# Kernel tuning notes

Hardware: AMD Instinct MI355X
Metric: run time of the kernel (lower is better)

The kernel has to match this reference:

```python
import jax, jax.numpy as jnp
import numpy as np

N, K, D, E, H = 65536, 8, 256, 256, 132  # points, components, latent_dim, encoder_dim, FC hidden

def setup_inputs() -> dict:
    key = jax.random.key(0)
    ks = jax.random.split(key, 12)
    s = 0.05
    f32 = jnp.float32
    return {
        "signal": jax.random.normal(ks[0], (N, E), f32),
        "components": jax.random.normal(ks[1], (K, N, D), f32),
        # message_map / update_map: Linear(D, D)
        "Wm": jax.random.normal(ks[2], (D, D), f32) * s,
        "bm": jnp.zeros((D,), f32),
        "Wu": jax.random.normal(ks[3], (D, D), f32) * s,
        "bu": jnp.zeros((D,), f32),
        "W0": jax.random.normal(ks[4], (H, E + D), f32) * s,
        "b0": jnp.zeros((H,), f32),
        "W1": jax.random.normal(ks[5], (H, H), f32) * s,
        "b1": jnp.zeros((H,), f32),
        "W2": jax.random.normal(ks[6], (H, H), f32) * s,
        "b2": jnpes if False else jnp.zeros((H,), f32),
        "W3": jax.random.normal(ks[7], (D, H), f32) * s,
        "b3": jnp.zeros((D,), f32),
    }

def reference(signal, components, Wm, bm, Wu, bu, W0, b0, W1, b1, W2, b2, W3, b3):
    k = components.shape[0]
    # sum_k Linear(comp_k) == Linear applied to sum, with bias counted k times (linearity)
    right = components.sum(0) @ Wm.T + k * bm          # [N, D]
    right = right @ Wu.T + bu                          # update_map
    x = jnp.concatenate([signal, right], axis=-1)      # [N, E+D]
    x = jax.nn.relu(x @ W0.T + b0)
    x = jax.nn.relu(x @ W1.T + b1)
    x = jax.nn.relu(x @ W2.T + b2)
    return x @ W3.T + b3                               # [N, D]
```

## Files before the change

kernel.cpp:

```cpp
#include <hip/hip_runtime.h>
#include <hip/hip_bf16.h>


typedef float  f32x4  __attribute__((ext_vector_type(4)));
typedef __bf16 bf16x8 __attribute__((ext_vector_type(8)));
typedef unsigned int   u32x2 __attribute__((ext_vector_type(2)));
typedef unsigned short u16x8 __attribute__((ext_vector_type(8)));

__device__ __forceinline__ unsigned short f2bf(float f) {
  unsigned int u = __builtin_bit_cast(unsigned int, f);
  u += 0x7fffu + ((u >> 16) & 1u);
  return (unsigned short)(u >> 16);
}

__device__ __forceinline__ u32x2 pack4(f32x4 v) {
  u32x2 r;
  r[0] = (unsigned)f2bf(v[0]) | ((unsigned)f2bf(v[1]) << 16);
  r[1] = (unsigned)f2bf(v[2]) | ((unsigned)f2bf(v[3]) << 16);
  return r;
}

__device__ __forceinline__ float wave_reduce(float s) {
#pragma unroll
  for (int m = 32; m > 0; m >>= 1) s += __shfl_xor(s, m, 64);
  return s;
}

__device__ __forceinline__ void gl16(const void* g, void* l) {
  __builtin_amdgcn_global_load_lds(
      (const __attribute__((address_space(1))) unsigned*)(unsigned long long)g,
      (__attribute__((address_space(3))) unsigned*)(unsigned)(unsigned long long)l,
      16, 0, 0);
}
__device__ __forceinline__ void gl4(const void* g, void* l) {
  __builtin_amdgcn_global_load_lds(
      (const __attribute__((address_space(1))) unsigned*)(unsigned long long)g,
      (__attribute__((address_space(3))) unsigned*)(unsigned)(unsigned long long)l,
      4, 0, 0);
}

__device__ __forceinline__ void stage10k(const char* src, char* dst,
                                         int wave, int lane) {
  const char* g0 = src + wave * 1024 + lane * 16;
  char* l0 = dst + wave * 1024;
  gl16(g0, l0);
  gl16(g0 + 4096, l0 + 4096);
  const char* g1 = src + 8192 + wave * 256 + lane * 4;
  char* l1 = dst + 8192 + wave * 256;
  gl4(g1, l1);
  gl4(g1 + 1024, l1 + 1024);
}
__device__ __forceinline__ void stage6k(const char* src, char* dst,
                                        int wave, int lane) {
  gl16(src + wave * 1024 + lane * 16, dst + wave * 1024);
  const char* g1 = src + 4096 + wave * 256 + lane * 4;
  char* l1 = dst + 4096 + wave * 256;
  gl4(g1, l1);
  gl4(g1 + 1024, l1 + 1024);
}

__global__ __launch_bounds__(256) void kA(const float* __restrict__ comp,
                                          const float* __restrict__ W0,
                                          const float* __restrict__ Wu,
                                          const float* __restrict__ bm,
                                          const float* __restrict__ bu,
                                          float* __restrict__ U,
                                          float* __restrict__ rb,
                                          unsigned short* __restrict__ csum) {
  const int b = blockIdx.x;
  if (b >= 196) {
    const int cb = b - 196;
    const int t = threadIdx.x;
    const f32x4* cp = (const f32x4*)comp;
    const size_t base = (size_t)cb * 2048 + t;
    f32x4 a[8];
#pragma unroll
    for (int j = 0; j < 8; ++j) a[j] = cp[base + j * 256];
#pragma unroll
    for (int k = 1; k < 8; ++k) {
      f32x4 t0[8];
#pragma unroll
      for (int j = 0; j < 8; ++j) t0[j] = cp[base + (size_t)k * 4194304u + j * 256];
#pragma unroll
      for (int j = 0; j < 8; ++j) a[j] += t0[j];
    }
    u32x2* op = (u32x2*)csum;
#pragma unroll
    for (int j = 0; j < 8; ++j) op[base + j * 256] = pack4(a[j]);
  } else if (b < 132) {
    const int h = b, d = threadIdx.x;
    float s = 0.f;
#pragma unroll 8
    for (int i = 0; i < 256; ++i) s += W0[h * 512 + 256 + i] * Wu[i * 256 + d];
    U[h * 256 + d] = s;
  } else {
    const int t = (b - 132) * 4 + (threadIdx.x >> 6);
    const int lane = threadIdx.x & 63;
    f32x4 w = ((const f32x4*)(Wu + t * 256))[lane];
    f32x4 v = ((const f32x4*)bm)[lane];
    float s = w[0] * v[0] + w[1] * v[1] + w[2] * v[2] + w[3] * v[3];
    s = wave_reduce(s);
    if (lane == 0) rb[t] = 8.f * s + bu[t];
  }
}

__global__ __launch_bounds__(256) void kB(const float* __restrict__ U,
                                          const float* __restrict__ Wm,
                                          const float* __restrict__ W0,
                                          const float* __restrict__ rb,
                                          const float* __restrict__ b0,
                                          const float* __restrict__ b1,
                                          const float* __restrict__ b2,
                                          float* __restrict__ Wc,
                                          float* __restrict__ bias1,
                                          float* __restrict__ b1p,
                                          float* __restrict__ b2p) {
  const int b = blockIdx.x;
  if (b < 132) {
    const int h = b, d = threadIdx.x;
    float s = 0.f;
#pragma unroll 8
    for (int j = 0; j < 256; ++j) s += U[h * 256 + j] * Wm[j * 256 + d];
    Wc[h * 256 + d] = s;
  } else {
    const int t = (b - 132) * 4 + (threadIdx.x >> 6);
    const int lane = threadIdx.x & 63;
    float v = 0.f;
    if (t < 132) {
      f32x4 w = ((const f32x4*)(W0 + t * 512 + 256))[lane];
      f32x4 r4 = ((const f32x4*)rb)[lane];
      float s = w[0] * r4[0] + w[1] * r4[1] + w[2] * r4[2] + w[3] * r4[3];
      s = wave_reduce(s);
      v = b0[t] + s;
    }
    if (lane == 0) {
      bias1[t] = v;
      b1p[t] = (t < 132) ? b1[t] : 0.f;
      b2p[t] = (t < 132) ? b2[t] : 0.f;
    }
  }
}

__global__ __launch_bounds__(256) void kC(
    const float* __restrict__ W0, const float* __restrict__ Wc,
    const float* __restrict__ W1, const float* __restrict__ W2,
    const float* __restrict__ W3,
    unsigned short* __restrict__ P1, unsigned short* __restrict__ P2,
    unsigned short* __restrict__ P3, unsigned short* __restrict__ P4) {
  int e = blockIdx.x * 256 + threadIdx.x;
  if (e >= 174080) return;
  unsigned short* dst; int NT, rel, mode;
  if (e < 81920)       { dst = P1; NT = 10; rel = e;          mode = 0; }
  else if (e < 107520) { dst = P2; NT = 10; rel = e - 81920;  mode = 1; }
  else if (e < 133120) { dst = P3; NT = 10; rel = e - 107520; mode = 2; }
  else                 { dst = P4; NT = 16; rel = e - 133120; mode = 3; }
  int chunk = rel >> 9, q = rel & 511;
  int lane = q >> 3, j = q & 7;
  int kk = chunk / NT, nt = chunk - kk * NT;
  int k = kk * 32 + (lane >> 4) * 8 + j;
  int n = nt * 16 + (lane & 15);
  float v = 0.f;
  if (mode == 0) {
    if (n < 132) v = (k < 256) ? W0[n * 512 + k] : Wc[n * 256 + (k - 256)];
  } else if (mode == 1) {
    if (n < 132 && k < 132) v = W1[n * 132 + k];
  } else if (mode == 2) {
    if (n < 132 && k < 132) v = W2[n * 132 + k];
  } else {
    if (k < 132) v = W3[n * 132 + k];
  }
  dst[rel] = f2bf(v);
}

__global__ __launch_bounds__(256, 3) void kD(
    const float* __restrict__ signal, const unsigned short* __restrict__ csum,
    const unsigned short* __restrict__ Pseq,
    const float* __restrict__ bias1, const float* __restrict__ b1p,
    const float* __restrict__ b2p, const float* __restrict__ b3,
    float* __restrict__ out) {
  extern __shared__ char lds[];
  const int tid = threadIdx.x;
  const int wave = tid >> 6;
  const int lane = tid & 63;
  const int lhalf = lane >> 4;
  const int l16 = lane & 15;
  char* act = lds + wave * 8192;
  char* wbA = lds + 32768;
  char* wbB = lds + 32768 + 10240;
  const char* Pb = (const char*)Pseq;
  const int row0 = ((int)blockIdx.x * 4 + wave) * 16;
  const int asw = (l16 & 7) << 4;

  f32x4 sg[16];
  const f32x4* sp = (const f32x4*)signal;
#pragma unroll
  for (int r = 0; r < 16; ++r) sg[r] = sp[(size_t)(row0 + r) * 64 + lane];
  u16x8 cs[8];
  const int r2 = lane >> 5, c32 = lane & 31;
#pragma unroll
  for (int j = 0; j < 8; ++j)
    cs[j] = *(const u16x8*)(csum + (size_t)(row0 + 2 * j + r2) * 256 + c32 * 8);

#pragma unroll
  for (int r = 0; r < 16; ++r)
    *(u32x2*)(act + r * 512 + ((lane * 8) ^ ((r & 7) << 4))) = pack4(sg[r]);

  stage10k(Pb, wbA, wave, lane);
  __syncthreads();

  f32x4 acc[10];
#pragma unroll
  for (int i = 0; i < 10; ++i) acc[i] = f32x4{0.f, 0.f, 0.f, 0.f};

#pragma unroll
  for (int kk = 0; kk < 8; ++kk) {
    stage10k(Pb + (kk + 1) * 10240, (((kk + 1) & 1) ? wbB : wbA), wave, lane);
    char* wb = (kk & 1) ? wbB : wbA;
    bf16x8 af = *(const bf16x8*)(act + l16 * 512 + ((kk * 64 + lhalf * 16) ^ asw));
#pragma unroll
    for (int nt = 0; nt < 10; ++nt)
      acc[nt] = __builtin_amdgcn_mfma_f32_16x16x32_bf16(
          af, *(const bf16x8*)(wb + nt * 1024 + lane * 16), acc[nt], 0, 0, 0);
    __syncthreads();
  }

  asm volatile("" ::: "memory");
#pragma unroll
  for (int j = 0; j < 8; ++j) {
    const int rw = 2 * j + r2;
    *(u16x8*)(act + rw * 512 + ((c32 * 16) ^ ((rw & 7) << 4))) = cs[j];
  }
  asm volatile("" ::: "memory");

#pragma unroll
  for (int kk = 8; kk < 16; ++kk) {
    if (kk < 15)
      stage10k(Pb + (kk + 1) * 10240, (((kk + 1) & 1) ? wbB : wbA), wave, lane);
    else
      stage10k(Pb + 163840, wbA, wave, lane);
    char* wb = (kk & 1) ? wbB : wbA;
    bf16x8 af =
        *(const bf16x8*)(act + l16 * 512 + (((kk - 8) * 64 + lhalf * 16) ^ asw));
#pragma unroll
    for (int nt = 0; nt < 10; ++nt)
      acc[nt] = __builtin_amdgcn_mfma_f32_16x16x32_bf16(
          af, *(const bf16x8*)(wb + nt * 1024 + lane * 16), acc[nt], 0, 0, 0);
    __syncthreads();
  }

  {
    float bv[10];
#pragma unroll
    for (int nt = 0; nt < 10; ++nt) bv[nt] = bias1[nt * 16 + l16];
    asm volatile("" ::: "memory");
#pragma unroll
    for (int nt = 0; nt < 10; ++nt) {
#pragma unroll
      for (int r = 0; r < 4; ++r) {
        const int row = lhalf * 4 + r;
        float v = fmaxf(acc[nt][r] + bv[nt], 0.f);
        *(unsigned short*)(act + row * 512 +
                           (((nt * 16 + l16) * 2) ^ ((row & 7) << 4))) = f2bf(v);
      }
    }
    asm volatile("" ::: "memory");
  }

#pragma unroll
  for (int L = 0; L < 2; ++L) {
    const char* hb = Pb + (L ? 215040 : 163840);
    const float* hbias = L ? b2p : b1p;
#pragma unroll
    for (int i = 0; i < 10; ++i) acc[i] = f32x4{0.f, 0.f, 0.f, 0.f};
#pragma unroll
    for (int kk = 0; kk < 5; ++kk) {
      const char* nsrc = (kk < 4) ? (hb + (kk + 1) * 10240)
                                  : (L ? (Pb + 266240) : (Pb + 215040));
      stage10k(nsrc, (((kk + L + 1) & 1) ? wbB : wbA), wave, lane);
      char* wb = ((kk + L) & 1) ? wbB : wbA;
      bf16x8 af =
          *(const bf16x8*)(act + l16 * 512 + ((kk * 64 + lhalf * 16) ^ asw));
#pragma unroll
      for (int nt = 0; nt < 10; ++nt)
        acc[nt] = __builtin_amdgcn_mfma_f32_16x16x32_bf16(
            af, *(const bf16x8*)(wb + nt * 1024 + lane * 16), acc[nt], 0, 0, 0);
      __syncthreads();
    }
    float bv[10];
#pragma unroll
    for (int nt = 0; nt < 10; ++nt) bv[nt] = hbias[nt * 16 + l16];
    asm volatile("" ::: "memory");
#pragma unroll
    for (int nt = 0; nt < 10; ++nt) {
#pragma unroll
      for (int r = 0; r < 4; ++r) {
        const int row = lhalf * 4 + r;
        float v = fmaxf(acc[nt][r] + bv[nt], 0.f);
        *(unsigned short*)(act + row * 512 +
                           (((nt * 16 + l16) * 2) ^ ((row & 7) << 4))) = f2bf(v);
      }
    }
    asm volatile("" ::: "memory");
  }

  f32x4 a4[16];
#pragma unroll
  for (int i = 0; i < 16; ++i) a4[i] = f32x4{0.f, 0.f, 0.f, 0.f};
  const char* P4b = Pb + 266240;
#pragma unroll
  for (int kk = 0; kk < 5; ++kk) {
    stage6k(P4b + kk * 16384 + 10240, wbB, wave, lane);
    bf16x8 af =
        *(const bf16x8*)(act + l16 * 512 + ((kk * 64 + lhalf * 16) ^ asw));
#pragma unroll
    for (int nt = 0; nt < 10; ++nt)
      a4[nt] = __builtin_amdgcn_mfma_f32_16x16x32_bf16(
          af, *(const bf16x8*)(wbA + nt * 1024 + lane * 16), a4[nt], 0, 0, 0);
    __syncthreads();
    if (kk < 4) stage10k(P4b + (kk + 1) * 16384, wbA, wave, lane);
#pragma unroll
    for (int nt = 10; nt < 16; ++nt)
      a4[nt] = __builtin_amdgcn_mfma_f32_16x16x32_bf16(
          af, *(const bf16x8*)(wbB + (nt - 10) * 1024 + lane * 16), a4[nt], 0, 0, 0);
    __syncthreads();
  }

  float bv[16];
#pragma unroll
  for (int nt = 0; nt < 16; ++nt) bv[nt] = b3[nt * 16 + l16];
  float* op = out + (size_t)(row0 + lhalf * 4) * 256 + l16;
#pragma unroll
  for (int nt = 0; nt < 16; ++nt) {
#pragma unroll
    for (int r = 0; r < 4; ++r)
      op[(size_t)r * 256 + nt * 16] = a4[nt][r] + bv[nt];
  }
}

extern "C" void kernel_launch(void* const* d_in, const int* in_sizes, int n_in,
                              void* d_out, int out_size, void* d_ws, size_t ws_size,
                              hipStream_t stream) {
  const float* signal = (const float*)d_in[0];
  const float* comp   = (const float*)d_in[1];
  const float* Wm = (const float*)d_in[2];
  const float* bm = (const float*)d_in[3];
  const float* Wu = (const float*)d_in[4];
  const float* bu = (const float*)d_in[5];
  const float* W0 = (const float*)d_in[6];
  const float* b0 = (const float*)d_in[7];
  const float* W1 = (const float*)d_in[8];
  const float* b1 = (const float*)d_in[9];
  const float* W2 = (const float*)d_in[10];
  const float* b2 = (const float*)d_in[11];
  const float* W3 = (const float*)d_in[12];
  const float* b3 = (const float*)d_in[13];

  char* ws = (char*)d_ws;
  float* U     = (float*)(ws + 0);
  float* Wc    = (float*)(ws + 135168);
  float* bias1 = (float*)(ws + 270336);
  float* b1p   = (float*)(ws + 270976);
  float* b2p   = (float*)(ws + 271616);
  float* rb    = (float*)(ws + 272256);
  unsigned short* P1 = (unsigned short*)(ws + 273408);
  unsigned short* P2 = (unsigned short*)(ws + 437248);
  unsigned short* P3 = (unsigned short*)(ws + 488448);
  unsigned short* P4 = (unsigned short*)(ws + 539648);
  unsigned short* csum = (unsigned short*)(ws + 621568);

  hipLaunchKernelGGL(kA, dim3(2244), dim3(256), 0, stream,
                     comp, W0, Wu, bm, bu, U, rb, csum);
  hipLaunchKernelGGL(kB, dim3(172), dim3(256), 0, stream,
                     U, Wm, W0, rb, b0, b1, b2, Wc, bias1, b1p, b2p);
  hipLaunchKernelGGL(kC, dim3(680), dim3(256), 0, stream,
                     W0, Wc, W1, W2, W3, P1, P2, P3, P4);
  hipLaunchKernelGGL(kD, dim3(1024), dim3(256), 53248, stream,
                     signal, csum, P1, bias1, b1p, b2p, b3, (float*)d_out);
}
```

Measured before the change: 190.7 us.

## Fuse component summation into main MLP kernel and merge weight-prep kernels

The sum over the 8 component tensors is moved out of the separate prep kernel and into the main MLP kernel. It is computed per row tile in registers and converted straight to bf16, so the intermediate bf16 csum buffer is never written to global memory and read back. The two weight-folding kernels are merged into one, with the intermediate results kept in shared memory, which removes a launch. Nontemporal loads and stores are used for the streamed inputs and the output. The risk is that the large component read now falls inside the occupancy-limited MFMA kernel, which may hide memory latency less well than a dedicated streaming kernel did.

```diff
diff --git a/kernel.cpp b/kernel.cpp
--- a/kernel.cpp
+++ b/kernel.cpp
@@ -18,12 +18,6 @@
   r[0] = (unsigned)f2bf(v[0]) | ((unsigned)f2bf(v[1]) << 16);
   r[1] = (unsigned)f2bf(v[2]) | ((unsigned)f2bf(v[3]) << 16);
   return r;
-}
-
-__device__ __forceinline__ float wave_reduce(float s) {
-#pragma unroll
-  for (int m = 32; m > 0; m >>= 1) s += __shfl_xor(s, m, 64);
-  return s;
 }
 
 __device__ __forceinline__ void gl16(const void* g, void* l) {
@@ -59,84 +53,55 @@
   gl4(g1 + 1024, l1 + 1024);
 }
 
-__global__ __launch_bounds__(256) void kA(const float* __restrict__ comp,
-                                          const float* __restrict__ W0,
-                                          const float* __restrict__ Wu,
-                                          const float* __restrict__ bm,
-                                          const float* __restrict__ bu,
-                                          float* __restrict__ U,
-                                          float* __restrict__ rb,
-                                          unsigned short* __restrict__ csum) {
+__global__ __launch_bounds__(256) void kP(
+    const float* __restrict__ W0, const float* __restrict__ Wu,
+    const float* __restrict__ Wm, const float* __restrict__ bm,
+    const float* __restrict__ bu, const float* __restrict__ b0,
+    const float* __restrict__ b1, const float* __restrict__ b2,
+    float* __restrict__ Wc, float* __restrict__ bias1,
+    float* __restrict__ b1p, float* __restrict__ b2p) {
   const int b = blockIdx.x;
-  if (b >= 196) {
-    const int cb = b - 196;
-    const int t = threadIdx.x;
-    const f32x4* cp = (const f32x4*)comp;
-    const size_t base = (size_t)cb * 2048 + t;
-    f32x4 a[8];
-#pragma unroll
-    for (int j = 0; j < 8; ++j) a[j] = cp[base + j * 256];
-#pragma unroll
-    for (int k = 1; k < 8; ++k) {
-      f32x4 t0[8];
-#pragma unroll
-      for (int j = 0; j < 8; ++j) t0[j] = cp[base + (size_t)k * 4194304u + j * 256];
-#pragma unroll
-      for (int j = 0; j < 8; ++j) a[j] += t0[j];
-    }
-    u32x2* op = (u32x2*)csum;
-#pragma unroll
-    for (int j = 0; j < 8; ++j) op[base + j * 256] = pack4(a[j]);
-  } else if (b < 132) {
-    const int h = b, d = threadIdx.x;
+  const int d = threadIdx.x;
+  if (b < 132) {
+    __shared__ float u[256];
+    const int h = b;
     float s = 0.f;
 #pragma unroll 8
     for (int i = 0; i < 256; ++i) s += W0[h * 512 + 256 + i] * Wu[i * 256 + d];
-    U[h * 256 + d] = s;
+    u[d] = s;
+    __syncthreads();
+    float s2 = 0.f;
+#pragma unroll 8
+    for (int j = 0; j < 256; ++j) s2 += u[j] * Wm[j * 256 + d];
+    Wc[h * 256 + d] = s2;
   } else {
-    const int t = (b - 132) * 4 + (threadIdx.x >> 6);
-    const int lane = threadIdx.x & 63;
-    f32x4 w = ((const f32x4*)(Wu + t * 256))[lane];
-    f32x4 v = ((const f32x4*)bm)[lane];
-    float s = w[0] * v[0] + w[1] * v[1] + w[2] * v[2] + w[3] * v[3];
-    s = wave_reduce(s);
-    if (lane == 0) rb[t] = 8.f * s + bu[t];
-  }
-}
-
-__global__ __launch_bounds__(256) void kB(const float* __restrict__ U,
-                                          const float* __restrict__ Wm,
-                                          const float* __restrict__ W0,
-                                          const float* __restrict__ rb,
-                                          const float* __restrict__ b0,
-                                          const float* __restrict__ b1,
-                                          const float* __restrict__ b2,
-                                          float* __restrict__ Wc,
-                                          float* __restrict__ bias1,
-                                          float* __restrict__ b1p,
-                                          float* __restrict__ b2p) {
-  const int b = blockIdx.x;
-  if (b < 132) {
-    const int h = b, d = threadIdx.x;
-    float s = 0.f;
+    __shared__ float bml[256];
+    __shared__ float rbl[256];
+    bml[d] = bm[d];
+    __syncthreads();
+    {
+      const f32x4* wr = (const f32x4*)(Wu + d * 256);
+      const f32x4* bm4 = (const f32x4*)bml;
+      float s = 0.f;
 #pragma unroll 8
-    for (int j = 0; j < 256; ++j) s += U[h * 256 + j] * Wm[j * 256 + d];
-    Wc[h * 256 + d] = s;
-  } else {
-    const int t = (b - 132) * 4 + (threadIdx.x >> 6);
-    const int lane = threadIdx.x & 63;
-    float v = 0.f;
-    if (t < 132) {
-      f32x4 w = ((const f32x4*)(W0 + t * 512 + 256))[lane];
-      f32x4 r4 = ((const f32x4*)rb)[lane];
-      float s = w[0] * r4[0] + w[1] * r4[1] + w[2] * r4[2] + w[3] * r4[3];
-      s = wave_reduce(s);
-      v = b0[t] + s;
-    }
-    if (lane == 0) {
-      bias1[t] = v;
-      b1p[t] = (t < 132) ? b1[t] : 0.f;
-      b2p[t] = (t < 132) ? b2[t] : 0.f;
+      for (int i = 0; i < 64; ++i) {
+        f32x4 w = wr[i], v = bm4[i];
+        s += w[0] * v[0] + w[1] * v[1] + w[2] * v[2] + w[3] * v[3];
+      }
+      rbl[d] = 8.f * s + bu[d];
+    }
+    __syncthreads();
+    if (d < 160) {
+      float v = 0.f;
+      if (d < 132) {
+        float s = 0.f;
+#pragma unroll 8
+        for (int j = 0; j < 256; ++j) s += W0[d * 512 + 256 + j] * rbl[j];
+        v = b0[d] + s;
+      }
+      bias1[d] = v;
+      b1p[d] = (d < 132) ? b1[d] : 0.f;
+      b2p[d] = (d < 132) ? b2[d] : 0.f;
     }
   }
 }
@@ -173,7 +138,7 @@
 }
 
 __global__ __launch_bounds__(256, 3) void kD(
-    const float* __restrict__ signal, const unsigned short* __restrict__ csum,
+    const float* __restrict__ signal, const float* __restrict__ comp,
     const unsigned short* __restrict__ Pseq,
     const float* __restrict__ bias1, const float* __restrict__ b1p,
     const float* __restrict__ b2p, const float* __restrict__ b3,
@@ -194,18 +159,49 @@
   f32x4 sg[16];
   const f32x4* sp = (const f32x4*)signal;
 #pragma unroll
-  for (int r = 0; r < 16; ++r) sg[r] = sp[(size_t)(row0 + r) * 64 + lane];
-  u16x8 cs[8];
-  const int r2 = lane >> 5, c32 = lane & 31;
-#pragma unroll
-  for (int j = 0; j < 8; ++j)
-    cs[j] = *(const u16x8*)(csum + (size_t)(row0 + 2 * j + r2) * 256 + c32 * 8);
-
+  for (int r = 0; r < 16; ++r)
+    sg[r] = __builtin_nontemporal_load(sp + (size_t)(row0 + r) * 64 + lane);
 #pragma unroll
   for (int r = 0; r < 16; ++r)
     *(u32x2*)(act + r * 512 + ((lane * 8) ^ ((r & 7) << 4))) = pack4(sg[r]);
 
   stage10k(Pb, wbA, wave, lane);
+
+  const int r2 = lane >> 5, c32 = lane & 31;
+  u16x8 cs[8];
+  const f32x4* cp = (const f32x4*)comp;
+#pragma unroll
+  for (int g = 0; g < 2; ++g) {
+    f32x4 a0[4], a1[4];
+#pragma unroll
+    for (int j = 0; j < 4; ++j) {
+      const size_t ix = (size_t)(row0 + 2 * (g * 4 + j) + r2) * 64 + c32 * 2;
+      a0[j] = __builtin_nontemporal_load(cp + ix);
+      a1[j] = __builtin_nontemporal_load(cp + ix + 1);
+    }
+#pragma unroll
+    for (int k = 1; k < 8; ++k) {
+      f32x4 t0[4], t1[4];
+#pragma unroll
+      for (int j = 0; j < 4; ++j) {
+        const size_t ix = (size_t)k * 4194304u +
+                          (size_t)(row0 + 2 * (g * 4 + j) + r2) * 64 + c32 * 2;
+        t0[j] = __builtin_nontemporal_load(cp + ix);
+        t1[j] = __builtin_nontemporal_load(cp + ix + 1);
+      }
+#pragma unroll
+      for (int j = 0; j < 4; ++j) { a0[j] += t0[j]; a1[j] += t1[j]; }
+    }
+#pragma unroll
+    for (int j = 0; j < 4; ++j) {
+      u16x8 v;
+      v[0] = f2bf(a0[j][0]); v[1] = f2bf(a0[j][1]);
+      v[2] = f2bf(a0[j][2]); v[3] = f2bf(a0[j][3]);
+      v[4] = f2bf(a1[j][0]); v[5] = f2bf(a1[j][1]);
+      v[6] = f2bf(a1[j][2]); v[7] = f2bf(a1[j][3]);
+      cs[g * 4 + j] = v;
+    }
+  }
   __syncthreads();
 
   f32x4 acc[10];
@@ -333,7 +329,8 @@
   for (int nt = 0; nt < 16; ++nt) {
 #pragma unroll
     for (int r = 0; r < 4; ++r)
-      op[(size_t)r * 256 + nt * 16] = a4[nt][r] + bv[nt];
+      __builtin_nontemporal_store(a4[nt][r] + bv[nt],
+                                  op + (size_t)r * 256 + nt * 16);
   }
 }
 
@@ -356,24 +353,19 @@
   const float* b3 = (const float*)d_in[13];
 
   char* ws = (char*)d_ws;
-  float* U     = (float*)(ws + 0);
-  float* Wc    = (float*)(ws + 135168);
-  float* bias1 = (float*)(ws + 270336);
-  float* b1p   = (float*)(ws + 270976);
-  float* b2p   = (float*)(ws + 271616);
-  float* rb    = (float*)(ws + 272256);
-  unsigned short* P1 = (unsigned short*)(ws + 273408);
-  unsigned short* P2 = (unsigned short*)(ws + 437248);
-  unsigned short* P3 = (unsigned short*)(ws + 488448);
-  unsigned short* P4 = (unsigned short*)(ws + 539648);
-  unsigned short* csum = (unsigned short*)(ws + 621568);
-
-  hipLaunchKernelGGL(kA, dim3(2244), dim3(256), 0, stream,
-                     comp, W0, Wu, bm, bu, U, rb, csum);
-  hipLaunchKernelGGL(kB, dim3(172), dim3(256), 0, stream,
-                     U, Wm, W0, rb, b0, b1, b2, Wc, bias1, b1p, b2p);
+  float* Wc    = (float*)(ws + 0);
+  float* bias1 = (float*)(ws + 135168);
+  float* b1p   = (float*)(ws + 135808);
+  float* b2p   = (float*)(ws + 136448);
+  unsigned short* P1 = (unsigned short*)(ws + 137216);
+  unsigned short* P2 = (unsigned short*)(ws + 301056);
+  unsigned short* P3 = (unsigned short*)(ws + 352256);
+  unsigned short* P4 = (unsigned short*)(ws + 403456);
+
+  hipLaunchKernelGGL(kP, dim3(133), dim3(256), 0, stream,
+                     W0, Wu, Wm, bm, bu, b0, b1, b2, Wc, bias1, b1p, b2p);
   hipLaunchKernelGGL(kC, dim3(680), dim3(256), 0, stream,
                      W0, Wc, W1, W2, W3, P1, P2, P3, P4);
   hipLaunchKernelGGL(kD, dim3(1024), dim3(256), 53248, stream,
-                     signal, csum, P1, bias1, b1p, b2p, b3, (float*)d_out);
-}
+                     signal, comp, P1, bias1, b1p, b2p, b3, (float*)d_out);
+}
```

After: 314.0 us. 1.65x slower.

## Load MLP weights directly into registers and process two row tiles per wave

Applied to the files above, without the earlier changes.

The fused MLP kernel no longer stages weight chunks through shared memory with block-wide barriers. Each wave now loads weight fragments straight from global memory into registers, double-buffered, and drops all __syncthreads. Each wave handles 32 rows instead of 16, so every loaded weight fragment feeds twice as many MFMAs. The grid is halved, LDS per block grows, and occupancy drops to 2 blocks per CU. This trades higher register pressure and more global/L2 traffic per wave for the removed barriers and LDS staging.

```diff
diff --git a/kernel.cpp b/kernel.cpp
--- a/kernel.cpp
+++ b/kernel.cpp
@@ -24,39 +24,6 @@
 #pragma unroll
   for (int m = 32; m > 0; m >>= 1) s += __shfl_xor(s, m, 64);
   return s;
-}
-
-__device__ __forceinline__ void gl16(const void* g, void* l) {
-  __builtin_amdgcn_global_load_lds(
-      (const __attribute__((address_space(1))) unsigned*)(unsigned long long)g,
-      (__attribute__((address_space(3))) unsigned*)(unsigned)(unsigned long long)l,
-      16, 0, 0);
-}
-__device__ __forceinline__ void gl4(const void* g, void* l) {
-  __builtin_amdgcn_global_load_lds(
-      (const __attribute__((address_space(1))) unsigned*)(unsigned long long)g,
-      (__attribute__((address_space(3))) unsigned*)(unsigned)(unsigned long long)l,
-      4, 0, 0);
-}
-
-__device__ __forceinline__ void stage10k(const char* src, char* dst,
-                                         int wave, int lane) {
-  const char* g0 = src + wave * 1024 + lane * 16;
-  char* l0 = dst + wave * 1024;
-  gl16(g0, l0);
-  gl16(g0 + 4096, l0 + 4096);
-  const char* g1 = src + 8192 + wave * 256 + lane * 4;
-  char* l1 = dst + 8192 + wave * 256;
-  gl4(g1, l1);
-  gl4(g1 + 1024, l1 + 1024);
-}
-__device__ __forceinline__ void stage6k(const char* src, char* dst,
-                                        int wave, int lane) {
-  gl16(src + wave * 1024 + lane * 16, dst + wave * 1024);
-  const char* g1 = src + 4096 + wave * 256 + lane * 4;
-  char* l1 = dst + 4096 + wave * 256;
-  gl4(g1, l1);
-  gl4(g1 + 1024, l1 + 1024);
 }
 
 __global__ __launch_bounds__(256) void kA(const float* __restrict__ comp,
@@ -172,7 +139,26 @@
   dst[rel] = f2bf(v);
 }
 
-__global__ __launch_bounds__(256, 3) void kD(
+#define WISS(BUF, CHUNK)                                                     \
+  {                                                                          \
+    _Pragma("unroll") for (int nt = 0; nt < 10; ++nt)                        \
+        BUF[nt] = *(const bf16x8*)(Pb + (CHUNK) * 10240 + nt * 1024 +        \
+                                   lane * 16);                               \
+  }
+#define WISS8L4(BUF, Q)                                                      \
+  {                                                                          \
+    _Pragma("unroll") for (int nt = 0; nt < 8; ++nt)                         \
+        BUF[nt] = *(const bf16x8*)(Pb + 266240 + ((Q) % 5) * 16384 +         \
+                                   ((Q) / 5) * 8192 + nt * 1024 + lane * 16);\
+  }
+#define MFMA10(ACC, BUF, AF)                                                 \
+  {                                                                          \
+    _Pragma("unroll") for (int nt = 0; nt < 10; ++nt)                        \
+        ACC[nt] = __builtin_amdgcn_mfma_f32_16x16x32_bf16(AF, BUF[nt],       \
+                                                          ACC[nt], 0, 0, 0); \
+  }
+
+__global__ __launch_bounds__(256, 2) void kD(
     const float* __restrict__ signal, const unsigned short* __restrict__ csum,
     const unsigned short* __restrict__ Pseq,
     const float* __restrict__ bias1, const float* __restrict__ b1p,
@@ -184,68 +170,86 @@
   const int lane = tid & 63;
   const int lhalf = lane >> 4;
   const int l16 = lane & 15;
-  char* act = lds + wave * 8192;
-  char* wbA = lds + 32768;
-  char* wbB = lds + 32768 + 10240;
+  const int r2 = lane >> 5, c32 = lane & 31;
+  char* act0 = lds + wave * 16384;
+  char* act1 = act0 + 8192;
   const char* Pb = (const char*)Pseq;
-  const int row0 = ((int)blockIdx.x * 4 + wave) * 16;
+  const int row0 = ((int)blockIdx.x * 4 + wave) * 32;
   const int asw = (l16 & 7) << 4;
-
-  f32x4 sg[16];
   const f32x4* sp = (const f32x4*)signal;
-#pragma unroll
-  for (int r = 0; r < 16; ++r) sg[r] = sp[(size_t)(row0 + r) * 64 + lane];
-  u16x8 cs[8];
-  const int r2 = lane >> 5, c32 = lane & 31;
+
+  {
+    f32x4 sg[16];
+#pragma unroll
+    for (int r = 0; r < 16; ++r) sg[r] = sp[(size_t)(row0 + r) * 64 + lane];
+#pragma unroll
+    for (int r = 0; r < 16; ++r)
+      *(u32x2*)(act0 + r * 512 + ((lane * 8) ^ ((r & 7) << 4))) = pack4(sg[r]);
+  }
+  {
+    f32x4 sg[16];
+#pragma unroll
+    for (int r = 0; r < 16; ++r)
+      sg[r] = sp[(size_t)(row0 + 16 + r) * 64 + lane];
+#pragma unroll
+    for (int r = 0; r < 16; ++r)
+      *(u32x2*)(act1 + r * 512 + ((lane * 8) ^ ((r & 7) << 4))) = pack4(sg[r]);
+  }
+
+  u16x8 cs0[8], cs1[8];
 #pragma unroll
   for (int j = 0; j < 8; ++j)
-    cs[j] = *(const u16x8*)(csum + (size_t)(row0 + 2 * j + r2) * 256 + c32 * 8);
-
-#pragma unroll
-  for (int r = 0; r < 16; ++r)
-    *(u32x2*)(act + r * 512 + ((lane * 8) ^ ((r & 7) << 4))) = pack4(sg[r]);
-
-  stage10k(Pb, wbA, wave, lane);
-  __syncthreads();
-
-  f32x4 acc[10];
-#pragma unroll
-  for (int i = 0; i < 10; ++i) acc[i] = f32x4{0.f, 0.f, 0.f, 0.f};
+    cs0[j] = *(const u16x8*)(csum + (size_t)(row0 + 2 * j + r2) * 256 + c32 * 8);
+#pragma unroll
+  for (int j = 0; j < 8; ++j)
+    cs1[j] =
+        *(const u16x8*)(csum + (size_t)(row0 + 16 + 2 * j + r2) * 256 + c32 * 8);
+
+  bf16x8 wA[10], wB[10];
+  WISS(wA, 0);
+
+  f32x4 acc0[10], acc1[10];
+#pragma unroll
+  for (int i = 0; i < 10; ++i) {
+    acc0[i] = f32x4{0.f, 0.f, 0.f, 0.f};
+    acc1[i] = f32x4{0.f, 0.f, 0.f, 0.f};
+  }
 
 #pragma unroll
   for (int kk = 0; kk < 8; ++kk) {
-    stage10k(Pb + (kk + 1) * 10240, (((kk + 1) & 1) ? wbB : wbA), wave, lane);
-    char* wb = (kk & 1) ? wbB : wbA;
-    bf16x8 af = *(const bf16x8*)(act + l16 * 512 + ((kk * 64 + lhalf * 16) ^ asw));
-#pragma unroll
-    for (int nt = 0; nt < 10; ++nt)
-      acc[nt] = __builtin_amdgcn_mfma_f32_16x16x32_bf16(
-          af, *(const bf16x8*)(wb + nt * 1024 + lane * 16), acc[nt], 0, 0, 0);
-    __syncthreads();
+    if ((kk + 1) & 1) { WISS(wB, kk + 1); } else { WISS(wA, kk + 1); }
+    bf16x8 af0 =
+        *(const bf16x8*)(act0 + l16 * 512 + ((kk * 64 + lhalf * 16) ^ asw));
+    bf16x8 af1 =
+        *(const bf16x8*)(act1 + l16 * 512 + ((kk * 64 + lhalf * 16) ^ asw));
+    if (kk & 1) {
+      MFMA10(acc0, wB, af0); MFMA10(acc1, wB, af1);
+    } else {
+      MFMA10(acc0, wA, af0); MFMA10(acc1, wA, af1);
+    }
   }
 
   asm volatile("" ::: "memory");
 #pragma unroll
   for (int j = 0; j < 8; ++j) {
     const int rw = 2 * j + r2;
-    *(u16x8*)(act + rw * 512 + ((c32 * 16) ^ ((rw & 7) << 4))) = cs[j];
+    *(u16x8*)(act0 + rw * 512 + ((c32 * 16) ^ ((rw & 7) << 4))) = cs0[j];
+    *(u16x8*)(act1 + rw * 512 + ((c32 * 16) ^ ((rw & 7) << 4))) = cs1[j];
   }
   asm volatile("" ::: "memory");
 
 #pragma unroll
   for (int kk = 8; kk < 16; ++kk) {
-    if (kk < 15)
-      stage10k(Pb + (kk + 1) * 10240, (((kk + 1) & 1) ? wbB : wbA), wave, lane);
-    else
-      stage10k(Pb + 163840, wbA, wave, lane);
-    char* wb = (kk & 1) ? wbB : wbA;
-    bf16x8 af =
-        *(const bf16x8*)(act + l16 * 512 + (((kk - 8) * 64 + lhalf * 16) ^ asw));
-#pragma unroll
-    for (int nt = 0; nt < 10; ++nt)
-      acc[nt] = __builtin_amdgcn_mfma_f32_16x16x32_bf16(
-          af, *(const bf16x8*)(wb + nt * 1024 + lane * 16), acc[nt], 0, 0, 0);
-    __syncthreads();
+    if ((kk + 1) & 1) { WISS(wB, kk + 1); } else { WISS(wA, kk + 1); }
+    bf16x8 af0 = *(const bf16x8*)(act0 + l16 * 512 +
+                                  (((kk - 8) * 64 + lhalf * 16) ^ asw));
+    bf16x8 af1 = *(const bf16x8*)(act1 + l16 * 512 +
+                                  (((kk - 8) * 64 + lhalf * 16) ^ asw));
+    if (kk & 1) {
+      MFMA10(acc0, wB, af0); MFMA10(acc1, wB, af1);
+    } else {
+      MFMA10(acc0, wA, af0); MFMA10(acc1, wA, af1);
+    }
   }
 
   {
@@ -258,33 +262,42 @@
 #pragma unroll
       for (int r = 0; r < 4; ++r) {
         const int row = lhalf * 4 + r;
-        float v = fmaxf(acc[nt][r] + bv[nt], 0.f);
-        *(unsigned short*)(act + row * 512 +
-                           (((nt * 16 + l16) * 2) ^ ((row & 7) << 4))) = f2bf(v);
+        const int off = (((nt * 16 + l16) * 2) ^ ((row & 7) << 4));
+        float v0 = fmaxf(acc0[nt][r] + bv[nt], 0.f);
+        float v1 = fmaxf(acc1[nt][r] + bv[nt], 0.f);
+        *(unsigned short*)(act0 + row * 512 + off) = f2bf(v0);
+        *(unsigned short*)(act1 + row * 512 + off) = f2bf(v1);
       }
     }
     asm volatile("" ::: "memory");
   }
 
+  bf16x8 w4A[8], w4B[8];
 #pragma unroll
   for (int L = 0; L < 2; ++L) {
-    const char* hb = Pb + (L ? 215040 : 163840);
     const float* hbias = L ? b2p : b1p;
 #pragma unroll
-    for (int i = 0; i < 10; ++i) acc[i] = f32x4{0.f, 0.f, 0.f, 0.f};
-#pragma unroll
-    for (int kk = 0; kk < 5; ++kk) {
-      const char* nsrc = (kk < 4) ? (hb + (kk + 1) * 10240)
-                                  : (L ? (Pb + 266240) : (Pb + 215040));
-      stage10k(nsrc, (((kk + L + 1) & 1) ? wbB : wbA), wave, lane);
-      char* wb = ((kk + L) & 1) ? wbB : wbA;
-      bf16x8 af =
-          *(const bf16x8*)(act + l16 * 512 + ((kk * 64 + lhalf * 16) ^ asw));
-#pragma unroll
-      for (int nt = 0; nt < 10; ++nt)
-        acc[nt] = __builtin_amdgcn_mfma_f32_16x16x32_bf16(
-            af, *(const bf16x8*)(wb + nt * 1024 + lane * 16), acc[nt], 0, 0, 0);
-      __syncthreads();
+    for (int i = 0; i < 10; ++i) {
+      acc0[i] = f32x4{0.f, 0.f, 0.f, 0.f};
+      acc1[i] = f32x4{0.f, 0.f, 0.f, 0.f};
+    }
+#pragma unroll
+    for (int qq = 0; qq < 5; ++qq) {
+      const int cc = 16 + L * 5 + qq;
+      if (cc < 25) {
+        if (cc & 1) { WISS(wA, cc + 1); } else { WISS(wB, cc + 1); }
+      } else {
+        WISS8L4(w4A, 0);
+      }
+      bf16x8 af0 =
+          *(const bf16x8*)(act0 + l16 * 512 + ((qq * 64 + lhalf * 16) ^ asw));
+      bf16x8 af1 =
+          *(const bf16x8*)(act1 + l16 * 512 + ((qq * 64 + lhalf * 16) ^ asw));
+      if (cc & 1) {
+        MFMA10(acc0, wB, af0); MFMA10(acc1, wB, af1);
+      } else {
+        MFMA10(acc0, wA, af0); MFMA10(acc1, wA, af1);
+      }
     }
     float bv[10];
 #pragma unroll
@@ -295,45 +308,62 @@
 #pragma unroll
       for (int r = 0; r < 4; ++r) {
         const int row = lhalf * 4 + r;
-        float v = fmaxf(acc[nt][r] + bv[nt], 0.f);
-        *(unsigned short*)(act + row * 512 +
-                           (((nt * 16 + l16) * 2) ^ ((row & 7) << 4))) = f2bf(v);
+        const int off = (((nt * 16 + l16) * 2) ^ ((row & 7) << 4));
+        float v0 = fmaxf(acc0[nt][r] + bv[nt], 0.f);
+        float v1 = fmaxf(acc1[nt][r] + bv[nt], 0.f);
+        *(unsigned short*)(act0 + row * 512 + off) = f2bf(v0);
+        *(unsigned short*)(act1 + row * 512 + off) = f2bf(v1);
       }
     }
     asm volatile("" ::: "memory");
   }
 
-  f32x4 a4[16];
-#pragma unroll
-  for (int i = 0; i < 16; ++i) a4[i] = f32x4{0.f, 0.f, 0.f, 0.f};
-  const char* P4b = Pb + 266240;
-#pragma unroll
-  for (int kk = 0; kk < 5; ++kk) {
-    stage6k(P4b + kk * 16384 + 10240, wbB, wave, lane);
-    bf16x8 af =
-        *(const bf16x8*)(act + l16 * 512 + ((kk * 64 + lhalf * 16) ^ asw));
-#pragma unroll
-    for (int nt = 0; nt < 10; ++nt)
-      a4[nt] = __builtin_amdgcn_mfma_f32_16x16x32_bf16(
-          af, *(const bf16x8*)(wbA + nt * 1024 + lane * 16), a4[nt], 0, 0, 0);
-    __syncthreads();
-    if (kk < 4) stage10k(P4b + (kk + 1) * 16384, wbA, wave, lane);
-#pragma unroll
-    for (int nt = 10; nt < 16; ++nt)
-      a4[nt] = __builtin_amdgcn_mfma_f32_16x16x32_bf16(
-          af, *(const bf16x8*)(wbB + (nt - 10) * 1024 + lane * 16), a4[nt], 0, 0, 0);
-    __syncthreads();
-  }
-
-  float bv[16];
-#pragma unroll
-  for (int nt = 0; nt < 16; ++nt) bv[nt] = b3[nt * 16 + l16];
-  float* op = out + (size_t)(row0 + lhalf * 4) * 256 + l16;
-#pragma unroll
-  for (int nt = 0; nt < 16; ++nt) {
-#pragma unroll
-    for (int r = 0; r < 4; ++r)
-      op[(size_t)r * 256 + nt * 16] = a4[nt][r] + bv[nt];
+#pragma unroll
+  for (int h = 0; h < 2; ++h) {
+    f32x4 a40[8], a41[8];
+#pragma unroll
+    for (int i = 0; i < 8; ++i) {
+      a40[i] = f32x4{0.f, 0.f, 0.f, 0.f};
+      a41[i] = f32x4{0.f, 0.f, 0.f, 0.f};
+    }
+#pragma unroll
+    for (int kk = 0; kk < 5; ++kk) {
+      const int q = h * 5 + kk;
+      if (q < 9) {
+        if (q & 1) { WISS8L4(w4A, q + 1); } else { WISS8L4(w4B, q + 1); }
+      }
+      bf16x8 af0 =
+          *(const bf16x8*)(act0 + l16 * 512 + ((kk * 64 + lhalf * 16) ^ asw));
+      bf16x8 af1 =
+          *(const bf16x8*)(act1 + l16 * 512 + ((kk * 64 + lhalf * 16) ^ asw));
+#pragma unroll
+      for (int i = 0; i < 8; ++i) {
+        if (q & 1) {
+          a40[i] = __builtin_amdgcn_mfma_f32_16x16x32_bf16(af0, w4B[i], a40[i],
+                                                           0, 0, 0);
+          a41[i] = __builtin_amdgcn_mfma_f32_16x16x32_bf16(af1, w4B[i], a41[i],
+                                                           0, 0, 0);
+        } else {
+          a40[i] = __builtin_amdgcn_mfma_f32_16x16x32_bf16(af0, w4A[i], a40[i],
+                                                           0, 0, 0);
+          a41[i] = __builtin_amdgcn_mfma_f32_16x16x32_bf16(af1, w4A[i], a41[i],
+                                                           0, 0, 0);
+        }
+      }
+    }
+    float bv[8];
+#pragma unroll
+    for (int i = 0; i < 8; ++i) bv[i] = b3[(h * 8 + i) * 16 + l16];
+    float* op0 = out + (size_t)(row0 + lhalf * 4) * 256 + h * 128 + l16;
+    float* op1 = out + (size_t)(row0 + 16 + lhalf * 4) * 256 + h * 128 + l16;
+#pragma unroll
+    for (int i = 0; i < 8; ++i) {
+#pragma unroll
+      for (int r = 0; r < 4; ++r) {
+        op0[(size_t)r * 256 + i * 16] = a40[i][r] + bv[i];
+        op1[(size_t)r * 256 + i * 16] = a41[i][r] + bv[i];
+      }
+    }
   }
 }
 
@@ -374,6 +404,6 @@
                      U, Wm, W0, rb, b0, b1, b2, Wc, bias1, b1p, b2p);
   hipLaunchKernelGGL(kC, dim3(680), dim3(256), 0, stream,
                      W0, Wc, W1, W2, W3, P1, P2, P3, P4);
-  hipLaunchKernelGGL(kD, dim3(1024), dim3(256), 53248, stream,
+  hipLaunchKernelGGL(kD, dim3(512), dim3(256), 65536, stream,
                      signal, csum, P1, bias1, b1p, b2p, b3, (float*)d_out);
 }
```

New measurement: 187.0 us (median of 2 runs). Within noise of the previous version (-1.9%).
